# Optimization experiments

Measured on AMD Instinct MI355X. Metric: run time of the kernel, lower is better.

## Reference

```python
import jax, jax.numpy as jnp
import numpy as np

D_MODEL, D_K, D_V = 512, 64, 64
B, S = 8, 4096


def setup_inputs() -> dict:
    key = jax.random.key(0)
    ks = jax.random.split(key, 10)
    scale = 1.0 / np.sqrt(D_MODEL)
    return {
        "q": jax.random.normal(ks[0], (B, S, D_MODEL), dtype=jnp.float32),
        "k": jax.random.normal(ks[1], (B, S, D_MODEL), dtype=jnp.float32),
        "v": jax.random.normal(ks[2], (B, S, D_MODEL), dtype=jnp.float32),
        "mask": jax.random.randint(ks[3], (B, S), 0, 2, dtype=jnp.int32),
        "Wq": jax.random.uniform(ks[4], (D_MODEL, D_K), jnp.float32, -scale, scale),
        "bq": jax.random.uniform(ks[5], (D_K,), jnp.float32, -scale, scale),
        "Wk": jax.random.uniform(ks[6], (D_MODEL, D_K), jnp.float32, -scale, scale),
        "bk": jax.random.uniform(ks[7], (D_K,), jnp.float32, -scale, scale),
        "Wv": jax.random.uniform(ks[8], (D_MODEL, D_V), jnp.float32, -scale, scale),
        "bv": jax.random.uniform(ks[9], (D_V,), jnp.float32, -scale, scale),
    }


def reference(q, k, v, mask, Wq, bq, Wk, bk, Wv, bv):
    # single-head QKV projections
    qh = jnp.einsum("bsd,dk->bsk", q, Wq) + bq  # [B,S,d_k]
    kh = jnp.einsum("bsd,dk->bsk", k, Wk) + bk  # [B,S,d_k]
    vh = jnp.einsum("bsd,dv->bsv", v, Wv) + bv  # [B,S,d_v]
    scores = jnp.einsum("bqk,bsk->bqs", qh, kh) / jnp.sqrt(jnp.float32(D_K))
    # key-padding mask: mask [B,S] -> [B,1,S], masked positions -> -1e10
    scores = jnp.where(mask[:, None, :] == 0, jnp.float32(-1e10), scores)
    attn = jax.nn.softmax(scores, axis=-1)
    return jnp.einsum("bqs,bsv->bqv", attn, vh)
```

## Files before the change

### kernel.cpp

```cpp
#include <hip/hip_runtime.h>

typedef __attribute__((ext_vector_type(8))) short bf16x8;
typedef __attribute__((ext_vector_type(4))) float f32x4;
typedef __attribute__((ext_vector_type(4))) unsigned short u16x4;

__device__ __forceinline__ short f2bf(float f) {
  unsigned int u = __builtin_bit_cast(unsigned int, f);
  u += 0x7fffu + ((u >> 16) & 1u);
  return (short)(u >> 16);
}

__global__ void prep_w(const float* __restrict__ Wq, const float* __restrict__ Wk,
                       const float* __restrict__ Wv, unsigned short* __restrict__ wt) {
  int idx = blockIdx.x * 256 + threadIdx.x;
  int m = idx >> 15;
  int rem = idx & 32767;
  int n = rem >> 9;
  int k = rem & 511;
  const float* W = (m == 0) ? Wq : ((m == 1) ? Wk : Wv);
  wt[idx] = (unsigned short)f2bf(W[k * 64 + n]);
}

__global__ __launch_bounds__(256, 3) void proj_kernel(
    const float* __restrict__ qx, const float* __restrict__ kx, const float* __restrict__ vx,
    const unsigned short* __restrict__ wt, const int* __restrict__ mask,
    const float* __restrict__ bqp, const float* __restrict__ bkp, const float* __restrict__ bvp,
    unsigned short* __restrict__ qo, unsigned short* __restrict__ ko,
    unsigned short* __restrict__ vo) {
  __shared__ unsigned short xs[16 * 512];
  __shared__ unsigned short wl[64 * 256];

  const int mode = blockIdx.y;
  const float* x = (mode == 0) ? qx : ((mode == 1) ? kx : vx);
  const float* bias = (mode == 0) ? bqp : ((mode == 1) ? bkp : bvp);
  const unsigned short* wtm = wt + mode * (64 * 512);
  const float osc = (mode == 0) ? 0.18033688011112042f : 1.0f;

  const int tid = threadIdx.x;
  const int w = tid >> 6, lane = tid & 63;
  const int g = lane >> 4, ln = lane & 15;
  const int rowbase = blockIdx.x * 16;

  {
    bf16x8 wreg[8];
#pragma unroll
    for (int i = 0; i < 8; ++i) {
      int c = tid + i * 256;
      int n = c >> 5, kc = c & 31;
      wreg[i] = *reinterpret_cast<const bf16x8*>(wtm + n * 512 + kc * 8);
    }
    const float* src = x + (size_t)rowbase * 512;
    float4 xr[8];
#pragma unroll
    for (int i = 0; i < 8; ++i) {
      int idx = i * 256 + tid;
      xr[i] = *reinterpret_cast<const float4*>(src + (size_t)idx * 4);
    }
#pragma unroll
    for (int i = 0; i < 8; ++i) {
      int c = tid + i * 256;
      int n = c >> 5, kc = c & 31;
      int bo = (n * 512 + kc * 16) ^ ((n & 7) << 4);
      *reinterpret_cast<bf16x8*>(reinterpret_cast<char*>(wl) + bo) = wreg[i];
    }
#pragma unroll
    for (int i = 0; i < 8; ++i) {
      int idx = i * 256 + tid;
      int row = idx >> 7, col4 = idx & 127;
      unsigned int pk0, pk1;
      asm("v_cvt_pk_bf16_f32 %0, %1, %2" : "=v"(pk0) : "v"(xr[i].x), "v"(xr[i].y));
      asm("v_cvt_pk_bf16_f32 %0, %1, %2" : "=v"(pk1) : "v"(xr[i].z), "v"(xr[i].w));
      union { unsigned int u[2]; u16x4 v; } pk;
      pk.u[0] = pk0;
      pk.u[1] = pk1;
      int u8 = col4 ^ ((row & 7) << 1);
      *reinterpret_cast<u16x4*>(reinterpret_cast<char*>(xs) + row * 1024 + u8 * 8) = pk.v;
    }
  }
  __syncthreads();

  const f32x4 fz = {0.f, 0.f, 0.f, 0.f};
  f32x4 acc = fz;

  const char* xrow_lds = reinterpret_cast<const char*>(xs) + ln * 1024;
  const int c7 = ln & 7;

#pragma unroll
  for (int t = 0; t < 16; ++t) {
    if (t == 8) {
      __syncthreads();
      bf16x8 wreg[8];
#pragma unroll
      for (int i = 0; i < 8; ++i) {
        int c = tid + i * 256;
        int n = c >> 5, kc = c & 31;
        wreg[i] = *reinterpret_cast<const bf16x8*>(wtm + n * 512 + 256 + kc * 8);
      }
#pragma unroll
      for (int i = 0; i < 8; ++i) {
        int c = tid + i * 256;
        int n = c >> 5, kc = c & 31;
        int bo = (n * 512 + kc * 16) ^ ((n & 7) << 4);
        *reinterpret_cast<bf16x8*>(reinterpret_cast<char*>(wl) + bo) = wreg[i];
      }
      __syncthreads();
    }
    int v = t * 4 + g;
    bf16x8 af = *reinterpret_cast<const bf16x8*>(xrow_lds + ((v ^ c7) * 16));
    int ks = t & 7;
    int n = w * 16 + ln;
    int bo = (n * 512 + ks * 64 + g * 16) ^ ((n & 7) << 4);
    bf16x8 bfrag = *reinterpret_cast<const bf16x8*>(reinterpret_cast<const char*>(wl) + bo);
    acc = __builtin_amdgcn_mfma_f32_16x16x32_bf16(af, bfrag, acc, 0, 0, 0);
  }

  const float bc = bias[w * 16 + ln];

  if (mode < 2) {
    unsigned short* o = (mode == 0) ? qo : ko;
#pragma unroll
    for (int r = 0; r < 4; ++r) {
      int row = rowbase + g * 4 + r;
      o[(size_t)row * 64 + w * 16 + ln] = (unsigned short)f2bf((acc[r] + bc) * osc);
    }
  } else {
    __syncthreads();
#pragma unroll
    for (int r = 0; r < 4; ++r)
      xs[(g * 4 + r) * 64 + w * 16 + ln] = (unsigned short)f2bf(acc[r] + bc);
    __syncthreads();
    int b = rowbase >> 12, s0 = rowbase & 4095;
    int dv = tid & 63, sc = tid >> 6;
    int sbase = s0 + sc * 4;
    const int* mrow = mask + b * 4096 + sbase;
    u16x4 pack;
#pragma unroll
    for (int j = 0; j < 4; ++j) {
      unsigned short vvv = xs[(sc * 4 + j) * 64 + dv];
      pack[j] = mrow[j] ? vvv : (unsigned short)0;
    }
    *reinterpret_cast<u16x4*>(vo + (size_t)(b * 64 + dv) * 4096 + sbase) = pack;
  }
}

#define KVBLK 128
#define NT 16

__global__ __launch_bounds__(256, 2) void attn_kernel(
    const unsigned short* __restrict__ qh, const unsigned short* __restrict__ kh,
    const unsigned short* __restrict__ vt, const int* __restrict__ mask,
    float* __restrict__ out0, float* __restrict__ out1,
    float* __restrict__ l0p, float* __restrict__ l1p) {
  __shared__ unsigned short kt[2][KVBLK * 64];
  __shared__ unsigned short vv[2][80 * 128];

  const int b = blockIdx.y;
  const int z = blockIdx.z;
  const int kv0 = z * (NT * KVBLK);
  float* __restrict__ optr = z ? out1 : out0;
  float* __restrict__ lptr = z ? l1p : l0p;
  const int qbase = blockIdx.x * 128;
  const int tid = threadIdx.x;
  const int w = tid >> 6, lane = tid & 63;
  const int g = lane >> 4, ln = lane & 15;

  for (int i = tid; i < 15 * 128; i += 256) {
    vv[0][65 * 128 + i] = 0;
    vv[1][65 * 128 + i] = 0;
  }

  bf16x8 qa[2][2];
#pragma unroll
  for (int qf = 0; qf < 2; ++qf) {
    int row = qbase + w * 32 + qf * 16 + ln;
    const unsigned short* qp = qh + (size_t)(b * 4096 + row) * 64;
    qa[qf][0] = *reinterpret_cast<const bf16x8*>(qp + g * 8);
    qa[qf][1] = *reinterpret_cast<const bf16x8*>(qp + 32 + g * 8);
  }

  const f32x4 fz = {0.f, 0.f, 0.f, 0.f};
  f32x4 accO[2][5];
#pragma unroll
  for (int qf = 0; qf < 2; ++qf)
#pragma unroll
    for (int nf = 0; nf < 5; ++nf) accO[qf][nf] = fz;

  const unsigned short* khb = kh + (size_t)b * 4096 * 64;
  const unsigned short* vtb = vt + (size_t)b * 64 * 4096;

  bf16x8 kreg[4], vreg[4];
  int mreg = 0;
  auto issue = [&](int ti) {
    int kvbase = kv0 + ti * KVBLK;
#pragma unroll
    for (int i = 0; i < 4; ++i) {
      int c = tid + i * 256;
      vreg[i] = *reinterpret_cast<const bf16x8*>(vtb + (size_t)(c >> 4) * 4096 + kvbase + (c & 15) * 8);
      kreg[i] = *reinterpret_cast<const bf16x8*>(khb + (size_t)(kvbase + (c >> 3)) * 64 + (c & 7) * 8);
    }
    if (tid < KVBLK) mreg = mask[b * 4096 + kvbase + tid];
  };
  auto commit = [&](int bs) {
#pragma unroll
    for (int i = 0; i < 4; ++i) {
      int c = tid + i * 256;
      int kbo = ((c >> 3) * 128 + (c & 7) * 16) ^ (((c >> 3) & 7) << 4);
      *reinterpret_cast<bf16x8*>(reinterpret_cast<char*>(kt[bs]) + kbo) = kreg[i];
      int dv = c >> 4;
      int P0 = (c & 15) * 8;
      int c2 = P0 >> 5, hh = (P0 >> 4) & 1, gg = (P0 >> 2) & 3;
      int x1 = 32 * c2 + 8 * gg + 4 * hh;
      int swz = (dv & 7) << 4;
      union { bf16x8 v; u16x4 h4[2]; } sp; sp.v = vreg[i];
      *reinterpret_cast<u16x4*>(reinterpret_cast<char*>(vv[bs]) + ((dv * 256 + 2 * x1) ^ swz)) = sp.h4[0];
      *reinterpret_cast<u16x4*>(reinterpret_cast<char*>(vv[bs]) + ((dv * 256 + 2 * x1 + 16) ^ swz)) = sp.h4[1];
    }
    if (tid < KVBLK) {
      int p = tid;
      int xx = 32 * (p >> 5) + 8 * ((p >> 2) & 3) + 4 * ((p >> 4) & 1) + (p & 3);
      vv[bs][64 * 128 + xx] = mreg ? (unsigned short)0x3F80 : (unsigned short)0;
    }
  };

  issue(0);
  commit(0);
  __syncthreads();
  int cur = 0;

  for (int ti = 0; ti < NT; ++ti) {
    if (ti + 1 < NT) issue(ti + 1);

    f32x4 s0[8], s1[8];
#pragma unroll
    for (int nf = 0; nf < 8; ++nf) { s0[nf] = fz; s1[nf] = fz; }
    __builtin_amdgcn_s_setprio(1);
#pragma unroll
    for (int c2 = 0; c2 < 2; ++c2)
#pragma unroll
      for (int nf = 0; nf < 8; ++nf) {
        int kvr = nf * 16 + ln;
        int bo = (kvr * 128 + c2 * 64 + g * 16) ^ ((kvr & 7) << 4);
        bf16x8 kf = *reinterpret_cast<const bf16x8*>(reinterpret_cast<const char*>(kt[cur]) + bo);
        s0[nf] = __builtin_amdgcn_mfma_f32_16x16x32_bf16(kf, qa[0][c2], s0[nf], 0, 0, 0);
        s1[nf] = __builtin_amdgcn_mfma_f32_16x16x32_bf16(kf, qa[1][c2], s1[nf], 0, 0, 0);
      }
    __builtin_amdgcn_s_setprio(0);

    unsigned int pw[2][4][4];
#pragma unroll
    for (int c2 = 0; c2 < 4; ++c2)
#pragma unroll
      for (int hh = 0; hh < 2; ++hh) {
        {
          float p0 = __builtin_exp2f(s0[2 * c2 + hh][0]);
          float p1 = __builtin_exp2f(s0[2 * c2 + hh][1]);
          float p2 = __builtin_exp2f(s0[2 * c2 + hh][2]);
          float p3 = __builtin_exp2f(s0[2 * c2 + hh][3]);
          unsigned int w0, w1;
          asm("v_cvt_pk_bf16_f32 %0, %1, %2" : "=v"(w0) : "v"(p0), "v"(p1));
          asm("v_cvt_pk_bf16_f32 %0, %1, %2" : "=v"(w1) : "v"(p2), "v"(p3));
          pw[0][c2][2 * hh] = w0;
          pw[0][c2][2 * hh + 1] = w1;
        }
        {
          float p0 = __builtin_exp2f(s1[2 * c2 + hh][0]);
          float p1 = __builtin_exp2f(s1[2 * c2 + hh][1]);
          float p2 = __builtin_exp2f(s1[2 * c2 + hh][2]);
          float p3 = __builtin_exp2f(s1[2 * c2 + hh][3]);
          unsigned int w0, w1;
          asm("v_cvt_pk_bf16_f32 %0, %1, %2" : "=v"(w0) : "v"(p0), "v"(p1));
          asm("v_cvt_pk_bf16_f32 %0, %1, %2" : "=v"(w1) : "v"(p2), "v"(p3));
          pw[1][c2][2 * hh] = w0;
          pw[1][c2][2 * hh + 1] = w1;
        }
      }

    __builtin_amdgcn_s_setprio(1);
#pragma unroll
    for (int c2 = 0; c2 < 4; ++c2) {
      union { unsigned int u[4]; bf16x8 v; } pa0, pa1;
#pragma unroll
      for (int t = 0; t < 4; ++t) { pa0.u[t] = pw[0][c2][t]; pa1.u[t] = pw[1][c2][t]; }
#pragma unroll
      for (int nf = 0; nf < 5; ++nf) {
        int dvr = nf * 16 + ln;
        int bo = (dvr * 256 + c2 * 64 + g * 16) ^ ((dvr & 7) << 4);
        bf16x8 vb = *reinterpret_cast<const bf16x8*>(reinterpret_cast<const char*>(vv[cur]) + bo);
        accO[0][nf] = __builtin_amdgcn_mfma_f32_16x16x32_bf16(pa0.v, vb, accO[0][nf], 0, 0, 0);
        accO[1][nf] = __builtin_amdgcn_mfma_f32_16x16x32_bf16(pa1.v, vb, accO[1][nf], 0, 0, 0);
      }
    }
    __builtin_amdgcn_s_setprio(0);

    if (ti + 1 < NT) commit(cur ^ 1);
    __syncthreads();
    cur ^= 1;
  }

#pragma unroll
  for (int qf = 0; qf < 2; ++qf)
#pragma unroll
    for (int r = 0; r < 4; ++r) {
      int grow = b * 4096 + qbase + w * 32 + qf * 16 + g * 4 + r;
#pragma unroll
      for (int nf = 0; nf < 4; ++nf)
        optr[(size_t)grow * 64 + nf * 16 + ln] = accO[qf][nf][r];
      if (ln == 0) lptr[grow] = accO[qf][4][r];
    }
}

__global__ __launch_bounds__(256) void combine_kernel(
    float* __restrict__ out, const float* __restrict__ po1,
    const float* __restrict__ l0p, const float* __restrict__ l1p) {
  int idx = blockIdx.x * 256 + threadIdx.x;
  int row = idx >> 4;
  float rl = 1.0f / (l0p[row] + l1p[row]);
  float4 a = reinterpret_cast<float4*>(out)[idx];
  float4 c = reinterpret_cast<const float4*>(po1)[idx];
  a.x = (a.x + c.x) * rl;
  a.y = (a.y + c.y) * rl;
  a.z = (a.z + c.z) * rl;
  a.w = (a.w + c.w) * rl;
  reinterpret_cast<float4*>(out)[idx] = a;
}

extern "C" void kernel_launch(void* const* d_in, const int* in_sizes, int n_in,
                              void* d_out, int out_size, void* d_ws, size_t ws_size,
                              hipStream_t stream) {
  const float* q = (const float*)d_in[0];
  const float* k = (const float*)d_in[1];
  const float* v = (const float*)d_in[2];
  const int* mask = (const int*)d_in[3];
  const float* Wq = (const float*)d_in[4];
  const float* bq = (const float*)d_in[5];
  const float* Wk = (const float*)d_in[6];
  const float* bk = (const float*)d_in[7];
  const float* Wv = (const float*)d_in[8];
  const float* bv = (const float*)d_in[9];

  char* wsb = (char*)d_ws;
  unsigned short* qh = (unsigned short*)(wsb);
  unsigned short* kh = (unsigned short*)(wsb + (4u << 20));
  unsigned short* vt = (unsigned short*)(wsb + (8u << 20));
  unsigned short* wt = (unsigned short*)(wsb + (12u << 20));
  float* po1 = (float*)(wsb + (12u << 20) + 196608);
  float* l0p = (float*)(wsb + (12u << 20) + 196608 + (8u << 20));
  float* l1p = l0p + 32768;

  prep_w<<<384, 256, 0, stream>>>(Wq, Wk, Wv, wt);
  proj_kernel<<<dim3(2048, 3), 256, 0, stream>>>(q, k, v, wt, mask, bq, bk, bv, qh, kh, vt);
  attn_kernel<<<dim3(32, 8, 2), 256, 0, stream>>>(qh, kh, vt, mask,
                                                  (float*)d_out, po1, l0p, l1p);
  combine_kernel<<<2048, 256, 0, stream>>>((float*)d_out, po1, l0p, l1p);
}
```

Measured before the change: 109.0 us.

## Make projection kernel persistent over row tiles with double-buffered input prefetch

Restructures the QKV projection kernel so each 512-thread block loads the full bf16 weight matrix into LDS once and then loops over four 32-row tiles. The next tile's fp32 input is prefetched into registers while the current tile's MFMAs run, with double-buffered LDS staging. This amortizes weight loading across more rows and overlaps global loads with compute. In exchange the grid shrinks to 768 blocks at one block per CU, and the larger LDS footprint limits occupancy.

```diff
diff --git a/kernel.cpp b/kernel.cpp
--- a/kernel.cpp
+++ b/kernel.cpp
@@ -21,14 +21,14 @@
   wt[idx] = (unsigned short)f2bf(W[k * 64 + n]);
 }
 
-__global__ __launch_bounds__(256, 3) void proj_kernel(
+__global__ __launch_bounds__(512, 1) void proj_kernel(
     const float* __restrict__ qx, const float* __restrict__ kx, const float* __restrict__ vx,
     const unsigned short* __restrict__ wt, const int* __restrict__ mask,
     const float* __restrict__ bqp, const float* __restrict__ bkp, const float* __restrict__ bvp,
     unsigned short* __restrict__ qo, unsigned short* __restrict__ ko,
     unsigned short* __restrict__ vo) {
-  __shared__ unsigned short xs[16 * 512];
-  __shared__ unsigned short wl[64 * 256];
+  __shared__ unsigned short wl[64 * 512];
+  __shared__ unsigned short xs[2][32 * 512];
 
   const int mode = blockIdx.y;
   const float* x = (mode == 0) ? qx : ((mode == 1) ? kx : vx);
@@ -39,33 +39,39 @@
   const int tid = threadIdx.x;
   const int w = tid >> 6, lane = tid & 63;
   const int g = lane >> 4, ln = lane & 15;
-  const int rowbase = blockIdx.x * 16;
+  const int rh = w & 1, h = w >> 1;
+  const int rowbase0 = blockIdx.x * 128;
 
   {
     bf16x8 wreg[8];
 #pragma unroll
     for (int i = 0; i < 8; ++i) {
-      int c = tid + i * 256;
-      int n = c >> 5, kc = c & 31;
+      int c = tid + i * 512;
+      int n = c >> 6, kc = c & 63;
       wreg[i] = *reinterpret_cast<const bf16x8*>(wtm + n * 512 + kc * 8);
     }
-    const float* src = x + (size_t)rowbase * 512;
-    float4 xr[8];
 #pragma unroll
     for (int i = 0; i < 8; ++i) {
-      int idx = i * 256 + tid;
+      int c = tid + i * 512;
+      int n = c >> 6, kc = c & 63;
+      int bo = n * 1024 + ((kc * 16) ^ ((n & 7) << 4));
+      *reinterpret_cast<bf16x8*>(reinterpret_cast<char*>(wl) + bo) = wreg[i];
+    }
+  }
+
+  float4 xr[8];
+  auto issue = [&](int st) {
+    const float* src = x + (size_t)(rowbase0 + st * 32) * 512;
+#pragma unroll
+    for (int i = 0; i < 8; ++i) {
+      int idx = i * 512 + tid;
       xr[i] = *reinterpret_cast<const float4*>(src + (size_t)idx * 4);
     }
+  };
+  auto commit = [&](int bs) {
 #pragma unroll
     for (int i = 0; i < 8; ++i) {
-      int c = tid + i * 256;
-      int n = c >> 5, kc = c & 31;
-      int bo = (n * 512 + kc * 16) ^ ((n & 7) << 4);
-      *reinterpret_cast<bf16x8*>(reinterpret_cast<char*>(wl) + bo) = wreg[i];
-    }
-#pragma unroll
-    for (int i = 0; i < 8; ++i) {
-      int idx = i * 256 + tid;
+      int idx = i * 512 + tid;
       int row = idx >> 7, col4 = idx & 127;
       unsigned int pk0, pk1;
       asm("v_cvt_pk_bf16_f32 %0, %1, %2" : "=v"(pk0) : "v"(xr[i].x), "v"(xr[i].y));
@@ -74,72 +80,64 @@
       pk.u[0] = pk0;
       pk.u[1] = pk1;
       int u8 = col4 ^ ((row & 7) << 1);
-      *reinterpret_cast<u16x4*>(reinterpret_cast<char*>(xs) + row * 1024 + u8 * 8) = pk.v;
-    }
-  }
+      *reinterpret_cast<u16x4*>(reinterpret_cast<char*>(&xs[bs][0]) + row * 1024 + u8 * 8) = pk.v;
+    }
+  };
+
+  issue(0);
+  commit(0);
   __syncthreads();
-
-  const f32x4 fz = {0.f, 0.f, 0.f, 0.f};
-  f32x4 acc = fz;
-
-  const char* xrow_lds = reinterpret_cast<const char*>(xs) + ln * 1024;
-  const int c7 = ln & 7;
-
-#pragma unroll
-  for (int t = 0; t < 16; ++t) {
-    if (t == 8) {
+  int cur = 0;
+
+  const float bc = bias[h * 16 + ln];
+  const int lrow = rh * 16 + ln;
+  const int c7 = lrow & 7;
+  const int n = h * 16 + ln;
+
+  for (int st = 0; st < 4; ++st) {
+    if (st < 4 - 1) issue(st + 1);
+
+    const f32x4 fz = {0.f, 0.f, 0.f, 0.f};
+    f32x4 acc = fz;
+    const char* xrow_lds = reinterpret_cast<const char*>(&xs[cur][0]) + lrow * 1024;
+#pragma unroll
+    for (int t = 0; t < 16; ++t) {
+      bf16x8 af = *reinterpret_cast<const bf16x8*>(xrow_lds + (((t * 4 + g) ^ c7) * 16));
+      int cb = n * 1024 + ((t * 64 + g * 16) ^ ((n & 7) << 4));
+      bf16x8 bfrag = *reinterpret_cast<const bf16x8*>(reinterpret_cast<const char*>(wl) + cb);
+      acc = __builtin_amdgcn_mfma_f32_16x16x32_bf16(af, bfrag, acc, 0, 0, 0);
+    }
+
+    int rowb = rowbase0 + st * 32;
+    if (mode < 2) {
+      unsigned short* o = (mode == 0) ? qo : ko;
+#pragma unroll
+      for (int r = 0; r < 4; ++r) {
+        int row = rowb + rh * 16 + g * 4 + r;
+        o[(size_t)row * 64 + h * 16 + ln] = (unsigned short)f2bf((acc[r] + bc) * osc);
+      }
+    } else {
       __syncthreads();
-      bf16x8 wreg[8];
-#pragma unroll
-      for (int i = 0; i < 8; ++i) {
-        int c = tid + i * 256;
-        int n = c >> 5, kc = c & 31;
-        wreg[i] = *reinterpret_cast<const bf16x8*>(wtm + n * 512 + 256 + kc * 8);
-      }
-#pragma unroll
-      for (int i = 0; i < 8; ++i) {
-        int c = tid + i * 256;
-        int n = c >> 5, kc = c & 31;
-        int bo = (n * 512 + kc * 16) ^ ((n & 7) << 4);
-        *reinterpret_cast<bf16x8*>(reinterpret_cast<char*>(wl) + bo) = wreg[i];
-      }
+#pragma unroll
+      for (int r = 0; r < 4; ++r)
+        xs[cur][(rh * 16 + g * 4 + r) * 64 + h * 16 + ln] = (unsigned short)f2bf(acc[r] + bc);
       __syncthreads();
-    }
-    int v = t * 4 + g;
-    bf16x8 af = *reinterpret_cast<const bf16x8*>(xrow_lds + ((v ^ c7) * 16));
-    int ks = t & 7;
-    int n = w * 16 + ln;
-    int bo = (n * 512 + ks * 64 + g * 16) ^ ((n & 7) << 4);
-    bf16x8 bfrag = *reinterpret_cast<const bf16x8*>(reinterpret_cast<const char*>(wl) + bo);
-    acc = __builtin_amdgcn_mfma_f32_16x16x32_bf16(af, bfrag, acc, 0, 0, 0);
-  }
-
-  const float bc = bias[w * 16 + ln];
-
-  if (mode < 2) {
-    unsigned short* o = (mode == 0) ? qo : ko;
-#pragma unroll
-    for (int r = 0; r < 4; ++r) {
-      int row = rowbase + g * 4 + r;
-      o[(size_t)row * 64 + w * 16 + ln] = (unsigned short)f2bf((acc[r] + bc) * osc);
-    }
-  } else {
+      int b = rowb >> 12, s0 = rowb & 4095;
+      int dv = tid & 63, sc = tid >> 6;
+      int sbase = s0 + sc * 4;
+      const int* mrow = mask + b * 4096 + sbase;
+      u16x4 pack;
+#pragma unroll
+      for (int j = 0; j < 4; ++j) {
+        unsigned short vvv = xs[cur][(sc * 4 + j) * 64 + dv];
+        pack[j] = mrow[j] ? vvv : (unsigned short)0;
+      }
+      *reinterpret_cast<u16x4*>(vo + (size_t)(b * 64 + dv) * 4096 + sbase) = pack;
+    }
+
+    if (st < 4 - 1) commit(cur ^ 1);
     __syncthreads();
-#pragma unroll
-    for (int r = 0; r < 4; ++r)
-      xs[(g * 4 + r) * 64 + w * 16 + ln] = (unsigned short)f2bf(acc[r] + bc);
-    __syncthreads();
-    int b = rowbase >> 12, s0 = rowbase & 4095;
-    int dv = tid & 63, sc = tid >> 6;
-    int sbase = s0 + sc * 4;
-    const int* mrow = mask + b * 4096 + sbase;
-    u16x4 pack;
-#pragma unroll
-    for (int j = 0; j < 4; ++j) {
-      unsigned short vvv = xs[(sc * 4 + j) * 64 + dv];
-      pack[j] = mrow[j] ? vvv : (unsigned short)0;
-    }
-    *reinterpret_cast<u16x4*>(vo + (size_t)(b * 64 + dv) * 4096 + sbase) = pack;
+    cur ^= 1;
   }
 }
 
@@ -348,7 +346,7 @@
   float* l1p = l0p + 32768;
 
   prep_w<<<384, 256, 0, stream>>>(Wq, Wk, Wv, wt);
-  proj_kernel<<<dim3(2048, 3), 256, 0, stream>>>(q, k, v, wt, mask, bq, bk, bv, qh, kh, vt);
+  proj_kernel<<<dim3(256, 3), 512, 0, stream>>>(q, k, v, wt, mask, bq, bk, bv, qh, kh, vt);
   attn_kernel<<<dim3(32, 8, 2), 256, 0, stream>>>(qh, kh, vt, mask,
                                                   (float*)d_out, po1, l0p, l1p);
   combine_kernel<<<2048, 256, 0, stream>>>((float*)d_out, po1, l0p, l1p);
```

New measurement: 108.3 us. Within noise of the previous version (-0.7%).
